# Performance work log

Measured on AMD Instinct MI355X. Metric: run time of the kernel, lower is better.

The kernel has to match this reference:

```python
import jax, jax.numpy as jnp
import numpy as np

DIM = 512
HEADS = 8
DIM_HEAD = 64
INNER = HEADS * DIM_HEAD
EPS = 1e-5


def setup_inputs() -> dict:
    key = jax.random.key(0)
    ks = jax.random.split(key, 8)
    x = jax.random.normal(ks[0], (4, 2048, DIM), dtype=jnp.float32)
    gamma = jnp.ones((DIM,), jnp.float32)
    beta = jnp.zeros((DIM,), jnp.float32)
    Wq = jax.random.normal(ks[1], (DIM, INNER), jnp.float32) / np.sqrt(DIM)
    Wkv = jax.random.normal(ks[2], (DIM, 2 * INNER), jnp.float32) / np.sqrt(DIM)
    mix_pre = jax.random.normal(ks[3], (HEADS, HEADS), jnp.float32)
    mix_post = jax.random.normal(ks[4], (HEADS, HEADS), jnp.float32)
    Wout = jax.random.normal(ks[5], (INNER, DIM), jnp.float32) / np.sqrt(INNER)
    bout = jnp.zeros((DIM,), jnp.float32)
    return {"x": x, "gamma": gamma, "beta": beta, "Wq": Wq, "Wkv": Wkv,
            "mix_pre": mix_pre, "mix_post": mix_post, "Wout": Wout, "bout": bout}


def reference(x, gamma, beta, Wq, Wkv, mix_pre, mix_post, Wout, bout):
    b, n, _ = x.shape
    scale = DIM_HEAD ** -0.5
    # LayerNorm
    mu = jnp.mean(x, axis=-1, keepdims=True)
    var = jnp.mean(jnp.square(x - mu), axis=-1, keepdims=True)
    xn = (x - mu) / jnp.sqrt(var + EPS) * gamma + beta
    # projections -> (b, h, n, d)
    q = (xn @ Wq).reshape(b, n, HEADS, DIM_HEAD).transpose(0, 2, 1, 3)
    kv = xn @ Wkv
    k, v = jnp.split(kv, 2, axis=-1)
    k = k.reshape(b, n, HEADS, DIM_HEAD).transpose(0, 2, 1, 3)
    v = v.reshape(b, n, HEADS, DIM_HEAD).transpose(0, 2, 1, 3)
    # talking-heads attention
    dots = jnp.einsum('bhid,bhjd->bhij', q, k) * scale
    dots = jnp.einsum('bhij,hg->bgij', dots, mix_pre)
    attn = jax.nn.softmax(dots, axis=-1)
    attn = jnp.einsum('bhij,hg->bgij', attn, mix_post)
    out = jnp.einsum('bhij,bhjd->bhid', attn, v)  # (b,h,n,d)
    out = out.transpose(0, 2, 1, 3).reshape(b, n, INNER)
    return out @ Wout + bout
```

## Files before the change

kernel.cpp:

```cpp
#include <hip/hip_runtime.h>

using short4_ = short     __attribute__((ext_vector_type(4)));
using short8  = short     __attribute__((ext_vector_type(8)));
using half2v  = _Float16  __attribute__((ext_vector_type(2)));
using half4   = _Float16  __attribute__((ext_vector_type(4)));
using float2_ = float     __attribute__((ext_vector_type(2)));
using float4_ = float     __attribute__((ext_vector_type(4)));

__device__ __forceinline__ unsigned short f2bf(float f) {
  union { float f; unsigned u; } v; v.f = f;
  unsigned r = v.u + 0x7fffu + ((v.u >> 16) & 1u);
  return (unsigned short)(r >> 16);
}
__device__ __forceinline__ float sgprf(float x) {
  return __int_as_float(__builtin_amdgcn_readfirstlane(__float_as_int(x)));
}
__device__ __forceinline__ half2v pkrtz(float a, float b) {
  return __builtin_bit_cast(half2v, __builtin_amdgcn_cvt_pkrtz(a, b));
}
__device__ __forceinline__ void bar_lds() {
  asm volatile("s_waitcnt lgkmcnt(0)\ns_barrier" ::: "memory");
}

__global__ __launch_bounds__(256, 4) void ln_kernel(
    const float* __restrict__ x, const float* __restrict__ gamma,
    const float* __restrict__ beta, unsigned short* __restrict__ xn) {
  int w = threadIdx.x >> 6, lane = threadIdx.x & 63;
  int row = blockIdx.x * 4 + w;
  const float4_* xr = (const float4_*)(x + row * 512);
  float4_ v0 = xr[lane * 2], v1 = xr[lane * 2 + 1];
  float s = 0.f, ss = 0.f;
#pragma unroll
  for (int e = 0; e < 4; ++e) { s += v0[e] + v1[e]; ss += v0[e]*v0[e] + v1[e]*v1[e]; }
#pragma unroll
  for (int off = 1; off < 64; off <<= 1) { s += __shfl_xor(s, off); ss += __shfl_xor(ss, off); }
  float mu = s * (1.f/512.f);
  float var = ss * (1.f/512.f) - mu*mu;
  float rs = rsqrtf(var + 1e-5f);
  const float4_* gp = (const float4_*)gamma;
  const float4_* bp = (const float4_*)beta;
  float4_ g0 = gp[lane*2], g1 = gp[lane*2+1], b0 = bp[lane*2], b1 = bp[lane*2+1];
  short8 pk;
#pragma unroll
  for (int e = 0; e < 4; ++e) {
    pk[e]   = (short)f2bf((v0[e]-mu)*rs*g0[e] + b0[e]);
    pk[e+4] = (short)f2bf((v1[e]-mu)*rs*g1[e] + b1[e]);
  }
  *(short8*)&xn[row*512 + lane*8] = pk;
}

__global__ __launch_bounds__(256, 4) void wconv(
    const float* __restrict__ Wq, const float* __restrict__ Wkv,
    const float* __restrict__ Wout,
    unsigned short* __restrict__ wt, unsigned short* __restrict__ wot) {
  int t = blockIdx.x * 256 + threadIdx.x;
  if (t < 786432) {
    int k = t / 1536, n = t % 1536;
    float v = (n < 512) ? Wq[k*512 + n] * 0.125f : Wkv[k*1024 + (n - 512)];
    wt[n*512 + k] = f2bf(v);
  } else {
    int t2 = t - 786432;
    int k = t2 >> 9, n = t2 & 511;
    wot[n*512 + k] = f2bf(Wout[k*512 + n]);
  }
}

__global__ __launch_bounds__(256, 2) void qkv_gemm(
    const unsigned short* __restrict__ A, const unsigned short* __restrict__ Bt,
    unsigned short* __restrict__ Qs, unsigned short* __restrict__ Kb,
    _Float16* __restrict__ Vt) {
  __shared__ unsigned short lA[128*32];
  __shared__ unsigned short lB[128*32];
  int bid = blockIdx.x;
  int tm = bid & 63, tn = bid >> 6;
  int m0 = tm * 128, n0 = tn * 128;
  int tid = threadIdx.x, lane = tid & 63, w = tid >> 6;
  int lrow = lane & 15, lgrp = lane >> 4;
  int wr = w >> 1, wc = w & 1;
  int r0 = tid >> 2, c0 = tid & 3;
  float4_ acc[4][4];
#pragma unroll
  for (int mi = 0; mi < 4; ++mi)
#pragma unroll
    for (int ni = 0; ni < 4; ++ni) acc[mi][ni] = (float4_){0.f,0.f,0.f,0.f};

  for (int k0 = 0; k0 < 512; k0 += 32) {
    short8 a0 = *(const short8*)&A[(m0 + r0)*512 + k0 + c0*8];
    short8 a1 = *(const short8*)&A[(m0 + 64 + r0)*512 + k0 + c0*8];
    short8 b0 = *(const short8*)&Bt[(n0 + r0)*512 + k0 + c0*8];
    short8 b1 = *(const short8*)&Bt[(n0 + 64 + r0)*512 + k0 + c0*8];
    __syncthreads();
    *(short8*)&lA[tid*8] = a0; *(short8*)&lA[(tid+256)*8] = a1;
    *(short8*)&lB[tid*8] = b0; *(short8*)&lB[(tid+256)*8] = b1;
    __syncthreads();
    short8 af[4], bfr[4];
#pragma unroll
    for (int mi = 0; mi < 4; ++mi) af[mi]  = *(const short8*)&lA[(wr*64 + mi*16 + lrow)*32 + lgrp*8];
#pragma unroll
    for (int ni = 0; ni < 4; ++ni) bfr[ni] = *(const short8*)&lB[(wc*64 + ni*16 + lrow)*32 + lgrp*8];
#pragma unroll
    for (int mi = 0; mi < 4; ++mi)
#pragma unroll
      for (int ni = 0; ni < 4; ++ni)
        acc[mi][ni] = __builtin_amdgcn_mfma_f32_16x16x32_bf16(af[mi], bfr[ni], acc[mi][ni], 0, 0, 0);
  }
#pragma unroll
  for (int mi = 0; mi < 4; ++mi) {
#pragma unroll
    for (int ni = 0; ni < 4; ++ni) {
      int col = n0 + wc*64 + ni*16 + lrow;
#pragma unroll
      for (int r = 0; r < 4; ++r) {
        int row = m0 + wr*64 + mi*16 + lgrp*4 + r;
        float v = acc[mi][ni][r];
        int b = row >> 11, i = row & 2047;
        if (col < 1024) {
          unsigned short* dst = (col < 512) ? Qs : Kb;
          int c = col & 511;
          dst[(((b<<3) + (c>>6))*2048 + i)*64 + (c & 63)] = f2bf(v);
        } else {
          int c = col - 1024;
          Vt[(((b<<3) + (c>>6))*64 + (c & 63))*2048 + i] = (_Float16)v;
        }
      }
    }
  }
}

__global__ __launch_bounds__(512, 4) void attn_f(
    const unsigned short* __restrict__ Qs, const unsigned short* __restrict__ Kb,
    const _Float16* __restrict__ Vt, const float* __restrict__ mixp,
    const float* __restrict__ mixq, unsigned short* __restrict__ AO) {
  __shared__ unsigned long long sbuf[2][8][64];
  __shared__ unsigned long long pbuf[2][8][64];
  int bid = blockIdx.x;
  int b = (bid & 7) >> 1;
  int it = ((bid >> 3) << 1) | (bid & 1);
  int i0 = it << 4;
  int tid = threadIdx.x, w = tid >> 6, lane = tid & 63;
  int lrow = lane & 15, lgrp = lane >> 4;
  int bh = (b << 3) + w;

  float mp[8];
#pragma unroll
  for (int h = 0; h < 8; ++h) mp[h] = sgprf(mixp[h*8 + w]);
  unsigned mqs[8];
#pragma unroll
  for (int g = 0; g < 8; ++g) {
    float v = mixq[g*8 + w];
    half2v h2 = pkrtz(v, v);
    mqs[g] = (unsigned)__builtin_amdgcn_readfirstlane((int)__builtin_bit_cast(unsigned, h2));
  }

  const unsigned short* qp = &Qs[(bh*2048 + i0 + lrow)*64 + lgrp*8];
  short8 qf0 = *(const short8*)qp;
  short8 qf1 = *(const short8*)(qp + 32);

  const unsigned short* kbase = &Kb[(bh*2048 + lrow)*64 + lgrp*8];
  const _Float16*       vbase = &Vt[(bh*64 + lrow)*2048 + lgrp*4];

  short8 ka0 = *(const short8*)kbase;
  short8 ka1 = *(const short8*)(kbase + 32);
  short8 kb0, kb1;

  float m_ = -1e30f, l_ = 0.f;

  auto p1body = [&](int t, short8& c0, short8& c1, short8& n0, short8& n1) {
    const unsigned short* kn = kbase + (((t + 1) & 127) << 10);
    n0 = *(const short8*)kn;
    n1 = *(const short8*)(kn + 32);
    float4_ S = {0.f,0.f,0.f,0.f};
    S = __builtin_amdgcn_mfma_f32_16x16x32_bf16(c0, qf0, S, 0, 0, 0);
    S = __builtin_amdgcn_mfma_f32_16x16x32_bf16(c1, qf1, S, 0, 0, 0);
    unsigned lo = __builtin_bit_cast(unsigned, pkrtz(S[0], S[1]));
    unsigned hi = __builtin_bit_cast(unsigned, pkrtz(S[2], S[3]));
    sbuf[t & 1][w][lane] = (unsigned long long)lo | ((unsigned long long)hi << 32);
    bar_lds();
    float s0 = 0.f, s1 = 0.f, s2 = 0.f, s3 = 0.f;
#pragma unroll
    for (int h = 0; h < 8; ++h) {
      unsigned long long u = sbuf[t & 1][h][lane];
      half2v l2 = __builtin_bit_cast(half2v, (unsigned)u);
      half2v h2 = __builtin_bit_cast(half2v, (unsigned)(u >> 32));
      s0 = fmaf(mp[h], (float)l2[0], s0);
      s1 = fmaf(mp[h], (float)l2[1], s1);
      s2 = fmaf(mp[h], (float)h2[0], s2);
      s3 = fmaf(mp[h], (float)h2[1], s3);
    }
    float tm = fmaxf(fmaxf(s0, s1), fmaxf(s2, s3));
    float mn = fmaxf(m_, tm);
    l_ = l_*__expf(m_-mn) + __expf(s0-mn) + __expf(s1-mn) + __expf(s2-mn) + __expf(s3-mn);
    m_ = mn;
  };
  for (int tt = 0; tt < 64; ++tt) {
    p1body(2*tt,     ka0, ka1, kb0, kb1);
    p1body(2*tt + 1, kb0, kb1, ka0, ka1);
  }
#pragma unroll
  for (int off = 16; off < 64; off <<= 1) {
    float om = __shfl_xor(m_, off);
    float ol = __shfl_xor(l_, off);
    float mn = fmaxf(m_, om);
    l_ = l_*__expf(m_-mn) + ol*__expf(om-mn);
    m_ = mn;
  }
  float mm = m_ + __logf(l_);

  float4_ ot0 = {0.f,0.f,0.f,0.f}, ot1 = ot0, ot2 = ot0, ot3 = ot0;
  auto p2body = [&](int t, short8& c0, short8& c1, short8& n0, short8& n1) {
    const unsigned short* kn = kbase + (((t + 1) & 127) << 10);
    n0 = *(const short8*)kn;
    n1 = *(const short8*)(kn + 32);
    const _Float16* vb = vbase + (t << 4);
    half4 vf0 = *(const half4*)vb;
    half4 vf1 = *(const half4*)(vb + 16*2048);
    half4 vf2 = *(const half4*)(vb + 32*2048);
    half4 vf3 = *(const half4*)(vb + 48*2048);
    float4_ S = {0.f,0.f,0.f,0.f};
    S = __builtin_amdgcn_mfma_f32_16x16x32_bf16(c0, qf0, S, 0, 0, 0);
    S = __builtin_amdgcn_mfma_f32_16x16x32_bf16(c1, qf1, S, 0, 0, 0);
    unsigned lo = __builtin_bit_cast(unsigned, pkrtz(S[0], S[1]));
    unsigned hi = __builtin_bit_cast(unsigned, pkrtz(S[2], S[3]));
    sbuf[t & 1][w][lane] = (unsigned long long)lo | ((unsigned long long)hi << 32);
    bar_lds();
    float s0 = 0.f, s1 = 0.f, s2 = 0.f, s3 = 0.f;
#pragma unroll
    for (int h = 0; h < 8; ++h) {
      unsigned long long u = sbuf[t & 1][h][lane];
      half2v l2 = __builtin_bit_cast(half2v, (unsigned)u);
      half2v h2 = __builtin_bit_cast(half2v, (unsigned)(u >> 32));
      s0 = fmaf(mp[h], (float)l2[0], s0);
      s1 = fmaf(mp[h], (float)l2[1], s1);
      s2 = fmaf(mp[h], (float)h2[0], s2);
      s3 = fmaf(mp[h], (float)h2[1], s3);
    }
    float p0 = __expf(s0 - mm), p1 = __expf(s1 - mm);
    float p2 = __expf(s2 - mm), p3 = __expf(s3 - mm);
    unsigned plo = __builtin_bit_cast(unsigned, pkrtz(p0, p1));
    unsigned phi = __builtin_bit_cast(unsigned, pkrtz(p2, p3));
    pbuf[t & 1][w][lane] = (unsigned long long)plo | ((unsigned long long)phi << 32);
    bar_lds();
    half2v A0 = (half2v)0, A1 = (half2v)0;
#pragma unroll
    for (int g = 0; g < 8; ++g) {
      unsigned long long u = pbuf[t & 1][g][lane];
      half2v l2 = __builtin_bit_cast(half2v, (unsigned)u);
      half2v h2 = __builtin_bit_cast(half2v, (unsigned)(u >> 32));
      half2v m2 = __builtin_bit_cast(half2v, mqs[g]);
      A0 += m2 * l2;
      A1 += m2 * h2;
    }
    half4 pb;
    pb[0] = A0[0]; pb[1] = A0[1]; pb[2] = A1[0]; pb[3] = A1[1];
    ot0 = __builtin_amdgcn_mfma_f32_16x16x16f16(vf0, pb, ot0, 0, 0, 0);
    ot1 = __builtin_amdgcn_mfma_f32_16x16x16f16(vf1, pb, ot1, 0, 0, 0);
    ot2 = __builtin_amdgcn_mfma_f32_16x16x16f16(vf2, pb, ot2, 0, 0, 0);
    ot3 = __builtin_amdgcn_mfma_f32_16x16x16f16(vf3, pb, ot3, 0, 0, 0);
  };
  for (int tt = 0; tt < 64; ++tt) {
    p2body(2*tt,     ka0, ka1, kb0, kb1);
    p2body(2*tt + 1, kb0, kb1, ka0, ka1);
  }

  unsigned short* ao = &AO[(b*2048 + i0 + lrow)*512 + w*64 + lgrp*4];
  float4_ ov[4] = {ot0, ot1, ot2, ot3};
#pragma unroll
  for (int dt = 0; dt < 4; ++dt) {
    short4_ pk;
#pragma unroll
    for (int r = 0; r < 4; ++r) pk[r] = (short)f2bf(ov[dt][r]);
    *(short4_*)(ao + dt*16) = pk;
  }
}

__global__ __launch_bounds__(256, 2) void out_gemm(
    const unsigned short* __restrict__ A, const unsigned short* __restrict__ Bt,
    const float* __restrict__ bout, float* __restrict__ out) {
  __shared__ unsigned short lA[128*32];
  __shared__ unsigned short lB[128*32];
  int bid = blockIdx.x;
  int tm = bid & 63, tn = bid >> 6;
  int m0 = tm * 128, n0 = tn * 128;
  int tid = threadIdx.x, lane = tid & 63, w = tid >> 6;
  int lrow = lane & 15, lgrp = lane >> 4;
  int wr = w >> 1, wc = w & 1;
  int r0 = tid >> 2, c0 = tid & 3;
  float4_ acc[4][4];
#pragma unroll
  for (int mi = 0; mi < 4; ++mi)
#pragma unroll
    for (int ni = 0; ni < 4; ++ni) acc[mi][ni] = (float4_){0.f,0.f,0.f,0.f};

  for (int k0 = 0; k0 < 512; k0 += 32) {
    short8 a0 = *(const short8*)&A[(m0 + r0)*512 + k0 + c0*8];
    short8 a1 = *(const short8*)&A[(m0 + 64 + r0)*512 + k0 + c0*8];
    short8 b0 = *(const short8*)&Bt[(n0 + r0)*512 + k0 + c0*8];
    short8 b1 = *(const short8*)&Bt[(n0 + 64 + r0)*512 + k0 + c0*8];
    __syncthreads();
    *(short8*)&lA[tid*8] = a0; *(short8*)&lA[(tid+256)*8] = a1;
    *(short8*)&lB[tid*8] = b0; *(short8*)&lB[(tid+256)*8] = b1;
    __syncthreads();
    short8 af[4], bfr[4];
#pragma unroll
    for (int mi = 0; mi < 4; ++mi) af[mi]  = *(const short8*)&lA[(wr*64 + mi*16 + lrow)*32 + lgrp*8];
#pragma unroll
    for (int ni = 0; ni < 4; ++ni) bfr[ni] = *(const short8*)&lB[(wc*64 + ni*16 + lrow)*32 + lgrp*8];
#pragma unroll
    for (int mi = 0; mi < 4; ++mi)
#pragma unroll
      for (int ni = 0; ni < 4; ++ni)
        acc[mi][ni] = __builtin_amdgcn_mfma_f32_16x16x32_bf16(af[mi], bfr[ni], acc[mi][ni], 0, 0, 0);
  }
#pragma unroll
  for (int mi = 0; mi < 4; ++mi)
#pragma unroll
    for (int ni = 0; ni < 4; ++ni) {
      int col = n0 + wc*64 + ni*16 + lrow;
      float bb = bout[col];
#pragma unroll
      for (int r = 0; r < 4; ++r) {
        int row = m0 + wr*64 + mi*16 + lgrp*4 + r;
        out[row*512 + col] = acc[mi][ni][r] + bb;
      }
    }
}

extern "C" void kernel_launch(void* const* d_in, const int* in_sizes, int n_in,
                              void* d_out, int out_size, void* d_ws, size_t ws_size,
                              hipStream_t stream) {
  (void)in_sizes; (void)n_in; (void)out_size; (void)ws_size;
  const float* x     = (const float*)d_in[0];
  const float* gamma = (const float*)d_in[1];
  const float* beta  = (const float*)d_in[2];
  const float* Wq    = (const float*)d_in[3];
  const float* Wkv   = (const float*)d_in[4];
  const float* mixp  = (const float*)d_in[5];
  const float* mixq  = (const float*)d_in[6];
  const float* Wout  = (const float*)d_in[7];
  const float* bout  = (const float*)d_in[8];
  float* out = (float*)d_out;

  unsigned short* xn  = (unsigned short*)d_ws;
  unsigned short* wt  = xn  + 4194304;
  unsigned short* wot = wt  + 786432;
  unsigned short* Qs  = wot + 262144;
  unsigned short* Kb  = Qs  + 4194304;
  _Float16*       Vt  = (_Float16*)(Kb + 4194304);
  unsigned short* AO  = (unsigned short*)(Vt + 4194304);

  ln_kernel<<<2048, 256, 0, stream>>>(x, gamma, beta, xn);
  wconv<<<4096, 256, 0, stream>>>(Wq, Wkv, Wout, wt, wot);
  qkv_gemm<<<768, 256, 0, stream>>>(xn, wt, Qs, Kb, Vt);
  attn_f<<<512, 512, 0, stream>>>(Qs, Kb, Vt, mixp, mixq, AO);
  out_gemm<<<256, 256, 0, stream>>>(AO, wot, bout, out);
}
```

Measured before the change: 580.8 us.

## Batch key tiles per barrier and software-pipeline post-mix stage in attention

Pass 1 now processes four key tiles per barrier instead of one, and pass 2 processes two. Pass 2 is also software-pipelined: the probability tile for the previous step is written to shared memory alongside the current scores, so a single barrier per step serves both the pre-mix and post-mix exchanges, with an epilogue that handles the final tile. The aim is to cut the number of workgroup barriers and raise instruction-level parallelism, at the cost of more registers and a larger shared-memory buffer.

```diff
diff --git a/kernel.cpp b/kernel.cpp
--- a/kernel.cpp
+++ b/kernel.cpp
@@ -17,6 +17,17 @@
 }
 __device__ __forceinline__ half2v pkrtz(float a, float b) {
   return __builtin_bit_cast(half2v, __builtin_amdgcn_cvt_pkrtz(a, b));
+}
+__device__ __forceinline__ half2v lo64(unsigned long long u) {
+  return __builtin_bit_cast(half2v, (unsigned)u);
+}
+__device__ __forceinline__ half2v hi64(unsigned long long u) {
+  return __builtin_bit_cast(half2v, (unsigned)(u >> 32));
+}
+__device__ __forceinline__ unsigned long long pk64(float a, float b, float c, float d) {
+  unsigned lo = __builtin_bit_cast(unsigned, pkrtz(a, b));
+  unsigned hi = __builtin_bit_cast(unsigned, pkrtz(c, d));
+  return (unsigned long long)lo | ((unsigned long long)hi << 32);
 }
 __device__ __forceinline__ void bar_lds() {
   asm volatile("s_waitcnt lgkmcnt(0)\ns_barrier" ::: "memory");
@@ -131,8 +142,7 @@
     const unsigned short* __restrict__ Qs, const unsigned short* __restrict__ Kb,
     const _Float16* __restrict__ Vt, const float* __restrict__ mixp,
     const float* __restrict__ mixq, unsigned short* __restrict__ AO) {
-  __shared__ unsigned long long sbuf[2][8][64];
-  __shared__ unsigned long long pbuf[2][8][64];
+  __shared__ unsigned long long lds[4096];
   int bid = blockIdx.x;
   int b = (bid & 7) >> 1;
   int it = ((bid >> 3) << 1) | (bid & 1);
@@ -155,120 +165,180 @@
   const unsigned short* qp = &Qs[(bh*2048 + i0 + lrow)*64 + lgrp*8];
   short8 qf0 = *(const short8*)qp;
   short8 qf1 = *(const short8*)(qp + 32);
-
   const unsigned short* kbase = &Kb[(bh*2048 + lrow)*64 + lgrp*8];
   const _Float16*       vbase = &Vt[(bh*64 + lrow)*2048 + lgrp*4];
 
-  short8 ka0 = *(const short8*)kbase;
-  short8 ka1 = *(const short8*)(kbase + 32);
-  short8 kb0, kb1;
-
   float m_ = -1e30f, l_ = 0.f;
 
-  auto p1body = [&](int t, short8& c0, short8& c1, short8& n0, short8& n1) {
-    const unsigned short* kn = kbase + (((t + 1) & 127) << 10);
-    n0 = *(const short8*)kn;
-    n1 = *(const short8*)(kn + 32);
-    float4_ S = {0.f,0.f,0.f,0.f};
-    S = __builtin_amdgcn_mfma_f32_16x16x32_bf16(c0, qf0, S, 0, 0, 0);
-    S = __builtin_amdgcn_mfma_f32_16x16x32_bf16(c1, qf1, S, 0, 0, 0);
-    unsigned lo = __builtin_bit_cast(unsigned, pkrtz(S[0], S[1]));
-    unsigned hi = __builtin_bit_cast(unsigned, pkrtz(S[2], S[3]));
-    sbuf[t & 1][w][lane] = (unsigned long long)lo | ((unsigned long long)hi << 32);
+  short8 kA[4][2], kB[4][2];
+#pragma unroll
+  for (int st = 0; st < 4; ++st) {
+    const unsigned short* kp = kbase + (st << 10);
+    kA[st][0] = *(const short8*)kp; kA[st][1] = *(const short8*)(kp + 32);
+  }
+  auto p1 = [&](int t, short8 (&kc)[4][2], short8 (&kn)[4][2]) {
+#pragma unroll
+    for (int st = 0; st < 4; ++st) {
+      const unsigned short* kp = kbase + ((((t + 1)*4 + st) & 127) << 10);
+      kn[st][0] = *(const short8*)kp; kn[st][1] = *(const short8*)(kp + 32);
+    }
+    int buf = (t & 1) << 11;
+#pragma unroll
+    for (int st = 0; st < 4; ++st) {
+      float4_ S = {0.f,0.f,0.f,0.f};
+      S = __builtin_amdgcn_mfma_f32_16x16x32_bf16(kc[st][0], qf0, S, 0, 0, 0);
+      S = __builtin_amdgcn_mfma_f32_16x16x32_bf16(kc[st][1], qf1, S, 0, 0, 0);
+      lds[buf + ((w*4 + st) << 6) + lane] = pk64(S[0], S[1], S[2], S[3]);
+    }
     bar_lds();
-    float s0 = 0.f, s1 = 0.f, s2 = 0.f, s3 = 0.f;
-#pragma unroll
-    for (int h = 0; h < 8; ++h) {
-      unsigned long long u = sbuf[t & 1][h][lane];
-      half2v l2 = __builtin_bit_cast(half2v, (unsigned)u);
-      half2v h2 = __builtin_bit_cast(half2v, (unsigned)(u >> 32));
-      s0 = fmaf(mp[h], (float)l2[0], s0);
-      s1 = fmaf(mp[h], (float)l2[1], s1);
-      s2 = fmaf(mp[h], (float)h2[0], s2);
-      s3 = fmaf(mp[h], (float)h2[1], s3);
-    }
-    float tm = fmaxf(fmaxf(s0, s1), fmaxf(s2, s3));
+    float sv[16];
+#pragma unroll
+    for (int st = 0; st < 4; ++st) {
+      float s0 = 0.f, s1 = 0.f, s2 = 0.f, s3 = 0.f;
+#pragma unroll
+      for (int h = 0; h < 8; ++h) {
+        unsigned long long u = lds[buf + ((h*4 + st) << 6) + lane];
+        half2v a = lo64(u), c = hi64(u);
+        s0 = fmaf(mp[h], (float)a[0], s0);
+        s1 = fmaf(mp[h], (float)a[1], s1);
+        s2 = fmaf(mp[h], (float)c[0], s2);
+        s3 = fmaf(mp[h], (float)c[1], s3);
+      }
+      sv[st*4+0] = s0; sv[st*4+1] = s1; sv[st*4+2] = s2; sv[st*4+3] = s3;
+    }
+    float tm = sv[0];
+#pragma unroll
+    for (int e = 1; e < 16; ++e) tm = fmaxf(tm, sv[e]);
     float mn = fmaxf(m_, tm);
-    l_ = l_*__expf(m_-mn) + __expf(s0-mn) + __expf(s1-mn) + __expf(s2-mn) + __expf(s3-mn);
+    float acc = 0.f;
+#pragma unroll
+    for (int e = 0; e < 16; ++e) acc += __expf(sv[e] - mn);
+    l_ = l_*__expf(m_ - mn) + acc;
     m_ = mn;
   };
-  for (int tt = 0; tt < 64; ++tt) {
-    p1body(2*tt,     ka0, ka1, kb0, kb1);
-    p1body(2*tt + 1, kb0, kb1, ka0, ka1);
-  }
+  for (int tt = 0; tt < 16; ++tt) { p1(2*tt, kA, kB); p1(2*tt + 1, kB, kA); }
+
 #pragma unroll
   for (int off = 16; off < 64; off <<= 1) {
     float om = __shfl_xor(m_, off);
     float ol = __shfl_xor(l_, off);
     float mn = fmaxf(m_, om);
-    l_ = l_*__expf(m_-mn) + ol*__expf(om-mn);
+    l_ = l_*__expf(m_ - mn) + ol*__expf(om - mn);
     m_ = mn;
   }
   float mm = m_ + __logf(l_);
 
-  float4_ ot0 = {0.f,0.f,0.f,0.f}, ot1 = ot0, ot2 = ot0, ot3 = ot0;
-  auto p2body = [&](int t, short8& c0, short8& c1, short8& n0, short8& n1) {
-    const unsigned short* kn = kbase + (((t + 1) & 127) << 10);
-    n0 = *(const short8*)kn;
-    n1 = *(const short8*)(kn + 32);
-    const _Float16* vb = vbase + (t << 4);
-    half4 vf0 = *(const half4*)vb;
-    half4 vf1 = *(const half4*)(vb + 16*2048);
-    half4 vf2 = *(const half4*)(vb + 32*2048);
-    half4 vf3 = *(const half4*)(vb + 48*2048);
-    float4_ S = {0.f,0.f,0.f,0.f};
-    S = __builtin_amdgcn_mfma_f32_16x16x32_bf16(c0, qf0, S, 0, 0, 0);
-    S = __builtin_amdgcn_mfma_f32_16x16x32_bf16(c1, qf1, S, 0, 0, 0);
-    unsigned lo = __builtin_bit_cast(unsigned, pkrtz(S[0], S[1]));
-    unsigned hi = __builtin_bit_cast(unsigned, pkrtz(S[2], S[3]));
-    sbuf[t & 1][w][lane] = (unsigned long long)lo | ((unsigned long long)hi << 32);
+  bar_lds();
+
+  float4_ ot[4];
+#pragma unroll
+  for (int dt = 0; dt < 4; ++dt) ot[dt] = (float4_){0.f,0.f,0.f,0.f};
+  short8 k2A[2][2], k2B[2][2];
+#pragma unroll
+  for (int st = 0; st < 2; ++st) {
+    const unsigned short* kp = kbase + (st << 10);
+    k2A[st][0] = *(const short8*)kp; k2A[st][1] = *(const short8*)(kp + 32);
+  }
+  unsigned long long pp0 = 0ull, pp1 = 0ull;
+
+  auto p2 = [&](int t, short8 (&kc)[2][2], short8 (&kn)[2][2]) {
+#pragma unroll
+    for (int st = 0; st < 2; ++st) {
+      const unsigned short* kp = kbase + ((((t + 1)*2 + st) & 127) << 10);
+      kn[st][0] = *(const short8*)kp; kn[st][1] = *(const short8*)(kp + 32);
+    }
+    half4 vf[2][4];
+#pragma unroll
+    for (int st = 0; st < 2; ++st) {
+      const _Float16* vb = vbase + (((2*t - 2 + st) & 127) << 4);
+#pragma unroll
+      for (int dt = 0; dt < 4; ++dt) vf[st][dt] = *(const half4*)(vb + dt*16*2048);
+    }
+    int sb = (t & 1) << 10;
+    int pbase = 2048 + ((t & 1) << 10);
+#pragma unroll
+    for (int st = 0; st < 2; ++st) {
+      float4_ S = {0.f,0.f,0.f,0.f};
+      S = __builtin_amdgcn_mfma_f32_16x16x32_bf16(kc[st][0], qf0, S, 0, 0, 0);
+      S = __builtin_amdgcn_mfma_f32_16x16x32_bf16(kc[st][1], qf1, S, 0, 0, 0);
+      lds[sb + ((w*2 + st) << 6) + lane] = pk64(S[0], S[1], S[2], S[3]);
+    }
+    lds[pbase + ((w*2 + 0) << 6) + lane] = pp0;
+    lds[pbase + ((w*2 + 1) << 6) + lane] = pp1;
     bar_lds();
-    float s0 = 0.f, s1 = 0.f, s2 = 0.f, s3 = 0.f;
-#pragma unroll
-    for (int h = 0; h < 8; ++h) {
-      unsigned long long u = sbuf[t & 1][h][lane];
-      half2v l2 = __builtin_bit_cast(half2v, (unsigned)u);
-      half2v h2 = __builtin_bit_cast(half2v, (unsigned)(u >> 32));
-      s0 = fmaf(mp[h], (float)l2[0], s0);
-      s1 = fmaf(mp[h], (float)l2[1], s1);
-      s2 = fmaf(mp[h], (float)h2[0], s2);
-      s3 = fmaf(mp[h], (float)h2[1], s3);
-    }
-    float p0 = __expf(s0 - mm), p1 = __expf(s1 - mm);
-    float p2 = __expf(s2 - mm), p3 = __expf(s3 - mm);
-    unsigned plo = __builtin_bit_cast(unsigned, pkrtz(p0, p1));
-    unsigned phi = __builtin_bit_cast(unsigned, pkrtz(p2, p3));
-    pbuf[t & 1][w][lane] = (unsigned long long)plo | ((unsigned long long)phi << 32);
+#pragma unroll
+    for (int st = 0; st < 2; ++st) {
+      float s0 = 0.f, s1 = 0.f, s2 = 0.f, s3 = 0.f;
+#pragma unroll
+      for (int h = 0; h < 8; ++h) {
+        unsigned long long u = lds[sb + ((h*2 + st) << 6) + lane];
+        half2v a = lo64(u), c = hi64(u);
+        s0 = fmaf(mp[h], (float)a[0], s0);
+        s1 = fmaf(mp[h], (float)a[1], s1);
+        s2 = fmaf(mp[h], (float)c[0], s2);
+        s3 = fmaf(mp[h], (float)c[1], s3);
+      }
+      unsigned long long np = pk64(__expf(s0 - mm), __expf(s1 - mm),
+                                   __expf(s2 - mm), __expf(s3 - mm));
+      if (st == 0) pp0 = np; else pp1 = np;
+    }
+    half2v A00 = (half2v)0, A01 = (half2v)0, A10 = (half2v)0, A11 = (half2v)0;
+#pragma unroll
+    for (int g = 0; g < 8; ++g) {
+      half2v m2 = __builtin_bit_cast(half2v, mqs[g]);
+      unsigned long long u0 = lds[pbase + ((g*2 + 0) << 6) + lane];
+      unsigned long long u1 = lds[pbase + ((g*2 + 1) << 6) + lane];
+      A00 += m2 * lo64(u0); A01 += m2 * hi64(u0);
+      A10 += m2 * lo64(u1); A11 += m2 * hi64(u1);
+    }
+    half4 pb0, pb1;
+    pb0[0] = A00[0]; pb0[1] = A00[1]; pb0[2] = A01[0]; pb0[3] = A01[1];
+    pb1[0] = A10[0]; pb1[1] = A10[1]; pb1[2] = A11[0]; pb1[3] = A11[1];
+#pragma unroll
+    for (int dt = 0; dt < 4; ++dt) {
+      ot[dt] = __builtin_amdgcn_mfma_f32_16x16x16f16(vf[0][dt], pb0, ot[dt], 0, 0, 0);
+      ot[dt] = __builtin_amdgcn_mfma_f32_16x16x16f16(vf[1][dt], pb1, ot[dt], 0, 0, 0);
+    }
+  };
+  for (int tt = 0; tt < 32; ++tt) { p2(2*tt, k2A, k2B); p2(2*tt + 1, k2B, k2A); }
+
+  {
+    int pbase = 2048;
+    lds[pbase + ((w*2 + 0) << 6) + lane] = pp0;
+    lds[pbase + ((w*2 + 1) << 6) + lane] = pp1;
+    half4 vf[2][4];
+#pragma unroll
+    for (int st = 0; st < 2; ++st) {
+      const _Float16* vb = vbase + ((126 + st) << 4);
+#pragma unroll
+      for (int dt = 0; dt < 4; ++dt) vf[st][dt] = *(const half4*)(vb + dt*16*2048);
+    }
     bar_lds();
-    half2v A0 = (half2v)0, A1 = (half2v)0;
+    half2v A00 = (half2v)0, A01 = (half2v)0, A10 = (half2v)0, A11 = (half2v)0;
 #pragma unroll
     for (int g = 0; g < 8; ++g) {
-      unsigned long long u = pbuf[t & 1][g][lane];
-      half2v l2 = __builtin_bit_cast(half2v, (unsigned)u);
-      half2v h2 = __builtin_bit_cast(half2v, (unsigned)(u >> 32));
       half2v m2 = __builtin_bit_cast(half2v, mqs[g]);
-      A0 += m2 * l2;
-      A1 += m2 * h2;
-    }
-    half4 pb;
-    pb[0] = A0[0]; pb[1] = A0[1]; pb[2] = A1[0]; pb[3] = A1[1];
-    ot0 = __builtin_amdgcn_mfma_f32_16x16x16f16(vf0, pb, ot0, 0, 0, 0);
-    ot1 = __builtin_amdgcn_mfma_f32_16x16x16f16(vf1, pb, ot1, 0, 0, 0);
-    ot2 = __builtin_amdgcn_mfma_f32_16x16x16f16(vf2, pb, ot2, 0, 0, 0);
-    ot3 = __builtin_amdgcn_mfma_f32_16x16x16f16(vf3, pb, ot3, 0, 0, 0);
-  };
-  for (int tt = 0; tt < 64; ++tt) {
-    p2body(2*tt,     ka0, ka1, kb0, kb1);
-    p2body(2*tt + 1, kb0, kb1, ka0, ka1);
+      unsigned long long u0 = lds[pbase + ((g*2 + 0) << 6) + lane];
+      unsigned long long u1 = lds[pbase + ((g*2 + 1) << 6) + lane];
+      A00 += m2 * lo64(u0); A01 += m2 * hi64(u0);
+      A10 += m2 * lo64(u1); A11 += m2 * hi64(u1);
+    }
+    half4 pb0, pb1;
+    pb0[0] = A00[0]; pb0[1] = A00[1]; pb0[2] = A01[0]; pb0[3] = A01[1];
+    pb1[0] = A10[0]; pb1[1] = A10[1]; pb1[2] = A11[0]; pb1[3] = A11[1];
+#pragma unroll
+    for (int dt = 0; dt < 4; ++dt) {
+      ot[dt] = __builtin_amdgcn_mfma_f32_16x16x16f16(vf[0][dt], pb0, ot[dt], 0, 0, 0);
+      ot[dt] = __builtin_amdgcn_mfma_f32_16x16x16f16(vf[1][dt], pb1, ot[dt], 0, 0, 0);
+    }
   }
 
   unsigned short* ao = &AO[(b*2048 + i0 + lrow)*512 + w*64 + lgrp*4];
-  float4_ ov[4] = {ot0, ot1, ot2, ot3};
 #pragma unroll
   for (int dt = 0; dt < 4; ++dt) {
     short4_ pk;
 #pragma unroll
-    for (int r = 0; r < 4; ++r) pk[r] = (short)f2bf(ov[dt][r]);
+    for (int r = 0; r < 4; ++r) pk[r] = (short)f2bf(ot[dt][r]);
     *(short4_*)(ao + dt*16) = pk;
   }
 }
```

After: 595.3 us. 1.02x slower.
